# Kernel optimization log

Measured on AMD Instinct MI355X. Metric: run time of the kernel, lower is better.

The kernel has to match this reference:

```python
import jax, jax.numpy as jnp
import numpy as np

N_WIRES = 4
N_OPS = 20  # depth * 10
DIM = 2 ** N_WIRES

_CNOT4 = jnp.array([[1, 0, 0, 0],
                    [0, 1, 0, 0],
                    [0, 0, 0, 1],
                    [0, 0, 1, 0]], dtype=jnp.complex64)


def _ry(t):
    c, s = jnp.cos(t / 2), jnp.sin(t / 2)
    return jnp.stack([jnp.stack([c, -s], -1), jnp.stack([s, c], -1)], -2).astype(jnp.complex64)


def _rx(t):
    c = jnp.cos(t / 2).astype(jnp.complex64)
    s = (-1j) * jnp.sin(t / 2).astype(jnp.complex64)
    return jnp.stack([jnp.stack([c, s], -1), jnp.stack([s, c], -1)], -2)


def _rz(t):
    e = jnp.exp(-0.5j * t.astype(jnp.complex64))
    z = jnp.zeros_like(e)
    return jnp.stack([jnp.stack([e, z], -1), jnp.stack([z, jnp.conj(e)], -1)], -2)


def _apply_1q(state, U, w):
    # state: [B, 2^n]; U: [2,2] (shared) or [B,2,2] (per-batch angle)
    b = state.shape[0]
    left, right = 2 ** w, 2 ** (N_WIRES - w - 1)
    s = state.reshape(b, left, 2, right)
    if U.ndim == 2:
        s = jnp.einsum('ij,bajc->baic', U, s)
    else:
        s = jnp.einsum('bij,bajc->baic', U, s)
    return s.reshape(b, -1)


def _apply_cnot(state, c):
    # CNOT on adjacent wires (c, c+1)
    b = state.shape[0]
    left, right = 2 ** c, 2 ** (N_WIRES - c - 2)
    s = state.reshape(b, left, 4, right)
    s = jnp.einsum('ij,bajc->baic', _CNOT4, s)
    return s.reshape(b, -1)


def _circuit(x, y, theta):
    b = x.shape[0]
    state = jnp.zeros((b, DIM), jnp.complex64).at[:, 0].set(1.0)
    # encoder: Ry(x_w) on each wire
    for w in range(N_WIRES):
        state = _apply_1q(state, _ry(x[:, w]), w)
    # fixed pseudo-random layer of 20 gates (RX/RY/RZ rotations + CNOTs)
    rot = (_rx, _ry, _rz)
    for i in range(N_OPS):
        kind = i % 4
        if kind == 3:
            state = _apply_cnot(state, (i // 4) % (N_WIRES - 1))
        else:
            w = (7 * i + 3) % N_WIRES
            state = _apply_1q(state, rot[kind](theta[i]), w)
    # second encoder: Ry(-y_w)
    for w in range(N_WIRES):
        state = _apply_1q(state, _ry(-y[:, w]), w)
    # PauliZ expectation on wire 0, then abs (original: abs(measure(...)[0]))
    probs = state.real ** 2 + state.imag ** 2  # [B, 16]
    p = probs.reshape(b, 2, -1)
    z0 = jnp.sum(p[:, 0], -1) - jnp.sum(p[:, 1], -1)
    return jnp.abs(z0)


def setup_inputs() -> dict:
    key = jax.random.key(0)
    k1, k2, k3 = jax.random.split(key, 3)
    B = 262144
    x = jax.random.normal(k1, (B, N_WIRES), jnp.float32)
    y = jax.random.normal(k2, (B, N_WIRES), jnp.float32)
    theta = jax.random.normal(k3, (N_OPS,), jnp.float32)
    return {"x": x, "y": y, "theta": theta}


def reference(x, y, theta):
    return _circuit(x, y, theta)
```

## Files before the change

### kernel.cpp

```cpp
#include <hip/hip_runtime.h>
#include <hip/hip_bf16.h>
#include <math.h>


template<int BIT>
__device__ __forceinline__ void rx8(float (&sr)[8], float (&si)[8], float c, float s) {
    #pragma unroll
    for (int i = 0; i < 8; ++i) {
        if (!(i & (1 << BIT))) {
            const int j = i | (1 << BIT);
            float ar = sr[i], ai = si[i], br = sr[j], bi = si[j];
            sr[i] = c * ar + s * bi;  si[i] = c * ai - s * br;
            sr[j] = c * br + s * ai;  si[j] = c * bi - s * ar;
        }
    }
}

template<int BIT>
__device__ __forceinline__ void ry8(float (&sr)[8], float (&si)[8], float c, float s) {
    #pragma unroll
    for (int i = 0; i < 8; ++i) {
        if (!(i & (1 << BIT))) {
            const int j = i | (1 << BIT);
            float ar = sr[i], ai = si[i], br = sr[j], bi = si[j];
            sr[i] = c * ar - s * br;  si[i] = c * ai - s * bi;
            sr[j] = s * ar + c * br;  si[j] = s * ai + c * bi;
        }
    }
}

template<int BIT>
__device__ __forceinline__ void rz8(float (&sr)[8], float (&si)[8], float c, float s) {
    #pragma unroll
    for (int i = 0; i < 8; ++i) {
        if (!(i & (1 << BIT))) {
            const int j = i | (1 << BIT);
            float ar = sr[i], ai = si[i], br = sr[j], bi = si[j];
            sr[i] = c * ar + s * ai;  si[i] = c * ai - s * ar;
            sr[j] = c * br - s * bi;  si[j] = c * bi + s * br;
        }
    }
}

template<int CB, int TB>
__device__ __forceinline__ void cnot8(float (&sr)[8], float (&si)[8]) {
    #pragma unroll
    for (int i = 0; i < 8; ++i) {
        if ((i & (1 << CB)) && !(i & (1 << TB))) {
            const int j = i | (1 << TB);
            float t;
            t = sr[i]; sr[i] = sr[j]; sr[j] = t;
            t = si[i]; si[i] = si[j]; si[j] = t;
        }
    }
}

__device__ __forceinline__ void x1_8(float (&sr)[8], float (&si)[8]) {
    #pragma unroll
    for (int i = 0; i < 4; ++i) {
        const int j = i + 4;
        float t;
        t = sr[i]; sr[i] = sr[j]; sr[j] = t;
        t = si[i]; si[i] = si[j]; si[j] = t;
    }
}

__device__ __forceinline__ void tri_transform(volatile float* T, int base, int s) {
    float x0 = T[base], x1 = T[base + s], x2 = T[base + 2 * s];
    T[base]         = 0.5f * (x0 + x2);
    T[base + s]     = 0.5f * (x0 - x2);
    T[base + 2 * s] = 0.5f * x1;
}

__global__ __launch_bounds__(256) void qfused_kernel(
        const float* __restrict__ x,
        const float* __restrict__ y,
        const float* __restrict__ theta,
        float* __restrict__ out,
        int B) {
    __shared__ float Vr[2][8][8], Vi[2][8][8];
    __shared__ float Nm[64];
    __shared__ float T[27];

    const int t = threadIdx.x;

    if (t < 16) {
        const int col = t & 7, blk = t >> 3;
        float sr[8], si[8];
        #pragma unroll
        for (int i = 0; i < 8; ++i) { sr[i] = (i == col) ? 1.0f : 0.0f; si[i] = 0.0f; }
        float tc, ts;
        #define ROT(IDX, FN, BIT) do { \
            __sincosf(0.5f * theta[IDX], &ts, &tc); \
            FN<BIT>(sr, si, tc, ts); \
        } while (0)
        ROT(0, rx8, 0); ROT(1, ry8, 1); ROT(2, rz8, 2);
        if (blk) x1_8(sr, si);
        ROT(4, rx8, 0); ROT(5, ry8, 1); ROT(6, rz8, 2);
        cnot8<2, 1>(sr, si);
        ROT(8, rx8, 0); ROT(9, ry8, 1); ROT(10, rz8, 2);
        cnot8<1, 0>(sr, si);
        ROT(12, rx8, 0); ROT(13, ry8, 1); ROT(14, rz8, 2);
        if (blk) x1_8(sr, si);
        ROT(16, rx8, 0); ROT(17, ry8, 1); ROT(18, rz8, 2);
        cnot8<2, 1>(sr, si);
        #undef ROT
        #pragma unroll
        for (int k = 0; k < 8; ++k) { Vr[blk][k][col] = sr[k]; Vi[blk][k][col] = si[k]; }
    }
    __syncthreads();

    if (t < 64) {
        const int i = t >> 3, j = t & 7;
        float a = 0.0f;
        #pragma unroll
        for (int k = 0; k < 8; ++k) {
            a = fmaf(Vr[0][k][i], Vr[1][k][j], a);
            a = fmaf(Vi[0][k][i], Vi[1][k][j], a);
        }
        Nm[t] = a;
    }
    __syncthreads();

    if (t < 27) {
        const int d1 = t / 9, d2 = (t / 3) % 3, d3 = t % 3;
        const int ones = ((d1 == 1) << 2) | ((d2 == 1) << 1) | (d3 == 1);
        const int twos = ((d1 == 2) << 2) | ((d2 == 2) << 1) | (d3 == 2);
        float a = 0.0f;
        #pragma unroll
        for (int c = 0; c < 8; ++c) {
            if (c & ~ones) continue;
            a += Nm[(twos | c) * 8 + (twos | (ones & ~c))];
        }
        T[t] = a;
    }
    __syncthreads();

    if (t < 9) tri_transform(T, t, 9);
    __syncthreads();
    if (t < 9) tri_transform(T, 9 * (t / 3) + (t % 3), 3);
    __syncthreads();
    if (t < 9) tri_transform(T, 3 * t, 1);
    __syncthreads();

    const int b = blockIdx.x * 256 + t;
    if (b >= B) return;

    float4 xv = reinterpret_cast<const float4*>(x)[b];
    float y0  = reinterpret_cast<const float4*>(y)[b].x;

    float cx0, sx0, cx1, sx1, cx2, sx2, cx3, sx3, cy, sy;
    __sincosf(xv.x, &sx0, &cx0);
    __sincosf(xv.y, &sx1, &cx1);
    __sincosf(xv.z, &sx2, &cx2);
    __sincosf(xv.w, &sx3, &cx3);
    __sincosf(y0,   &sy,  &cy);

    float r3[9];
    #pragma unroll
    for (int m = 0; m < 9; ++m)
        r3[m] = fmaf(sx3, T[3 * m + 2], fmaf(cx3, T[3 * m + 1], T[3 * m]));
    float r2[3];
    #pragma unroll
    for (int m = 0; m < 3; ++m)
        r2[m] = fmaf(sx2, r3[3 * m + 2], fmaf(cx2, r3[3 * m + 1], r3[3 * m]));
    float g = fmaf(sx1, r2[2], fmaf(cx1, r2[1], r2[0]));

    out[b] = fabsf(fmaf(cy, cx0, sy * sx0 * g));
}

extern "C" void kernel_launch(void* const* d_in, const int* in_sizes, int n_in,
                              void* d_out, int out_size, void* d_ws, size_t ws_size,
                              hipStream_t stream) {
    const float* x     = (const float*)d_in[0];
    const float* y     = (const float*)d_in[1];
    const float* theta = (const float*)d_in[2];
    float* out = (float*)d_out;

    int B = out_size;
    int block = 256;
    int grid = (B + block - 1) / block;
    qfused_kernel<<<grid, block, 0, stream>>>(x, y, theta, out, B);
}
```

Measured before the change: 9.765 us.

## Hoist input loads and theta trig before setup; fold first layer analytically

Moves the per-thread x/y global loads to the kernel start, clamping the index for out-of-range threads, so their latency overlaps the shared-memory setup phase. All threads now compute the cos/sin of the twelve theta angles up front. The first rotation layer is applied in closed form to the basis column, and the two X gates are folded into the initial row index and the final store index, which also drops the trailing CNOT. This shortens the serial prologue, at the cost of redundant trig work in every thread and a subtle rewrite of the gate sequence that has to stay equivalent.

```diff
diff --git a/kernel.cpp b/kernel.cpp
--- a/kernel.cpp
+++ b/kernel.cpp
@@ -55,16 +55,6 @@
     }
 }
 
-__device__ __forceinline__ void x1_8(float (&sr)[8], float (&si)[8]) {
-    #pragma unroll
-    for (int i = 0; i < 4; ++i) {
-        const int j = i + 4;
-        float t;
-        t = sr[i]; sr[i] = sr[j]; sr[j] = t;
-        t = si[i]; si[i] = si[j]; si[j] = t;
-    }
-}
-
 __device__ __forceinline__ void tri_transform(volatile float* T, int base, int s) {
     float x0 = T[base], x1 = T[base + s], x2 = T[base + 2 * s];
     T[base]         = 0.5f * (x0 + x2);
@@ -83,30 +73,59 @@
     __shared__ float T[27];
 
     const int t = threadIdx.x;
+    const int b = blockIdx.x * 256 + t;
+    const int bc = (b < B) ? b : (B - 1);
+
+    const float4 xv = reinterpret_cast<const float4*>(x)[bc];
+    const float  y0 = y[4 * bc];
+
+    float tC[12], tS[12];
+    #pragma unroll
+    for (int i = 0; i < 12; ++i) {
+        const int idx = i + (i / 3);
+        const float th = 0.5f * theta[idx];
+        tC[i] = __cosf(th);
+        tS[i] = __sinf(th);
+    }
 
     if (t < 16) {
         const int col = t & 7, blk = t >> 3;
+        const int c0 = col & 1, c1 = (col >> 1) & 1, c2 = (col >> 2) & 1;
         float sr[8], si[8];
         #pragma unroll
-        for (int i = 0; i < 8; ++i) { sr[i] = (i == col) ? 1.0f : 0.0f; si[i] = 0.0f; }
-        float tc, ts;
-        #define ROT(IDX, FN, BIT) do { \
-            __sincosf(0.5f * theta[IDX], &ts, &tc); \
-            FN<BIT>(sr, si, tc, ts); \
-        } while (0)
-        ROT(0, rx8, 0); ROT(1, ry8, 1); ROT(2, rz8, 2);
-        if (blk) x1_8(sr, si);
-        ROT(4, rx8, 0); ROT(5, ry8, 1); ROT(6, rz8, 2);
+        for (int i = 0; i < 8; ++i) { sr[i] = 0.0f; si[i] = 0.0f; }
+        {
+            const float pr = tC[2];
+            const float pi = c2 ? tS[2] : -tS[2];
+            const int r2s = (c2 ^ blk) << 2;
+            #pragma unroll
+            for (int r1 = 0; r1 < 2; ++r1) {
+                const float g = (r1 == c1) ? tC[1] : (r1 ? tS[1] : -tS[1]);
+                #pragma unroll
+                for (int r0 = 0; r0 < 2; ++r0) {
+                    const int r = r2s | (r1 << 1) | r0;
+                    if (r0 == c0) { sr[r] = pr * g * tC[0]; si[r] = pi * g * tC[0]; }
+                    else          { sr[r] = pi * g * tS[0]; si[r] = -pr * g * tS[0]; }
+                }
+            }
+        }
+        rx8<0>(sr, si, tC[3], tS[3]);
+        ry8<1>(sr, si, tC[4], tS[4]);
+        rz8<2>(sr, si, tC[5], tS[5]);
         cnot8<2, 1>(sr, si);
-        ROT(8, rx8, 0); ROT(9, ry8, 1); ROT(10, rz8, 2);
+        rx8<0>(sr, si, tC[6], tS[6]);
+        ry8<1>(sr, si, tC[7], tS[7]);
+        rz8<2>(sr, si, tC[8], tS[8]);
         cnot8<1, 0>(sr, si);
-        ROT(12, rx8, 0); ROT(13, ry8, 1); ROT(14, rz8, 2);
-        if (blk) x1_8(sr, si);
-        ROT(16, rx8, 0); ROT(17, ry8, 1); ROT(18, rz8, 2);
-        cnot8<2, 1>(sr, si);
-        #undef ROT
+        rx8<0>(sr, si, tC[9], tS[9]);
+        ry8<1>(sr, si, tC[10], tS[10]);
+        rz8<2>(sr, si, tC[11], tS[11]);
+        const int rxr = blk << 2;
         #pragma unroll
-        for (int k = 0; k < 8; ++k) { Vr[blk][k][col] = sr[k]; Vi[blk][k][col] = si[k]; }
+        for (int k = 0; k < 8; ++k) {
+            Vr[blk][k ^ rxr][col] = sr[k];
+            Vi[blk][k ^ rxr][col] = si[k];
+        }
     }
     __syncthreads();
 
@@ -143,18 +162,13 @@
     if (t < 9) tri_transform(T, 3 * t, 1);
     __syncthreads();
 
-    const int b = blockIdx.x * 256 + t;
     if (b >= B) return;
 
-    float4 xv = reinterpret_cast<const float4*>(x)[b];
-    float y0  = reinterpret_cast<const float4*>(y)[b].x;
-
-    float cx0, sx0, cx1, sx1, cx2, sx2, cx3, sx3, cy, sy;
-    __sincosf(xv.x, &sx0, &cx0);
-    __sincosf(xv.y, &sx1, &cx1);
-    __sincosf(xv.z, &sx2, &cx2);
-    __sincosf(xv.w, &sx3, &cx3);
-    __sincosf(y0,   &sy,  &cy);
+    const float cx0 = __cosf(xv.x), sx0 = __sinf(xv.x);
+    const float cx1 = __cosf(xv.y), sx1 = __sinf(xv.y);
+    const float cx2 = __cosf(xv.z), sx2 = __sinf(xv.z);
+    const float cx3 = __cosf(xv.w), sx3 = __sinf(xv.w);
+    const float cy  = __cosf(y0),   sy  = __sinf(y0);
 
     float r3[9];
     #pragma unroll
@@ -164,7 +178,7 @@
     #pragma unroll
     for (int m = 0; m < 3; ++m)
         r2[m] = fmaf(sx2, r3[3 * m + 2], fmaf(cx2, r3[3 * m + 1], r3[3 * m]));
-    float g = fmaf(sx1, r2[2], fmaf(cx1, r2[1], r2[0]));
+    const float g = fmaf(sx1, r2[2], fmaf(cx1, r2[1], r2[0]));
 
     out[b] = fabsf(fmaf(cy, cx0, sy * sx0 * g));
 }
```

Result: slower. 11.24 us (+15.1%).
